# Kernel tuning notes

Measured on AMD Instinct MI355X. Metric: run time of the kernel, lower is better.

## Reference

```python
import jax, jax.numpy as jnp
import numpy as np

B, S, H = 4, 2048, 512
E, K = 8, 2
DFF = 4 * H


def setup_inputs() -> dict:
    key = jax.random.key(0)
    ks = jax.random.split(key, 6)
    x = jax.random.normal(ks[0], (B, S, H), dtype=jnp.float32)
    gate_W = jax.random.normal(ks[1], (H, E), dtype=jnp.float32) * 0.02
    gate_b = jnp.zeros((E,), dtype=jnp.float32)
    # Stacked expert params; Linear stored as [in, out] so y = x @ W + b
    W1 = jax.random.normal(ks[2], (E, H, DFF), dtype=jnp.float32) * 0.02
    b1 = jnp.zeros((E, DFF), dtype=jnp.float32)
    W2 = jax.random.normal(ks[3], (E, DFF, H), dtype=jnp.float32) * 0.02
    b2 = jnp.zeros((E, H), dtype=jnp.float32)
    return {"x": x, "gate_W": gate_W, "gate_b": gate_b,
            "W1": W1, "b1": b1, "W2": W2, "b2": b2}


def reference(x, gate_W, gate_b, W1, b1, W2, b2):
    bsz, seq, hid = x.shape
    flat = x.reshape(-1, hid)                       # [T, H]
    T = flat.shape[0]
    gate_logits = flat @ gate_W + gate_b            # [T, E]
    topk_vals, topk_idx = jax.lax.top_k(gate_logits, K)   # [T, K]
    topk_w = jax.nn.softmax(topk_vals, axis=-1)      # softmax over selected logits only

    # Scatter top-k weights into a dense per-token combine matrix [T, E];
    # zero weight where a token is not routed -> identical math to masked dispatch.
    combine = jnp.zeros((T, E), dtype=flat.dtype).at[
        jnp.arange(T)[:, None], topk_idx].add(topk_w)

    out_flat = jnp.zeros_like(flat)
    for e in range(E):  # fixed small loop over structurally distinct experts
        h = jax.nn.gelu(flat @ W1[e] + b1[e], approximate=False) @ W2[e] + b2[e]
        out_flat = out_flat + h * combine[:, e:e + 1]
    out = out_flat.reshape(bsz, seq, hid)

    probs = jax.nn.softmax(gate_logits, axis=-1).mean(axis=0)   # [E]
    l_aux = jnp.sum(probs * probs) * E
    expert_counts = jnp.zeros((E,), dtype=jnp.float32).at[
        topk_idx.reshape(-1)].add(1.0)
    return out, l_aux, expert_counts
```

## Files before the change

### kernel.cpp

```cpp
#include <hip/hip_runtime.h>
#include <math.h>

#define TOK 8192
#define HD  512
#define NE  8
#define DFF 2048

typedef __attribute__((ext_vector_type(8))) short bf16x8;
typedef __attribute__((ext_vector_type(4))) float floatx4;

__device__ inline unsigned short f2bf(float f) {
    union { float f; unsigned u; } v; v.f = f;
    unsigned r = v.u + 0x7FFFu + ((v.u >> 16) & 1u);
    return (unsigned short)(r >> 16);
}

__device__ inline float gelu_exact(float v) {
    return 0.5f * v * (1.f + erff(v * 0.70710678118654752f));
}

typedef __attribute__((address_space(1))) const unsigned int glb_u32;
typedef __attribute__((address_space(3))) unsigned int lds_u32;
__device__ __forceinline__ void gload16(const unsigned short* g, unsigned short* l) {
    __builtin_amdgcn_global_load_lds((glb_u32*)g, (lds_u32*)l, 16, 0, 0);
}

__global__ __launch_bounds__(256) void prep_kernel(
    const float* __restrict__ x, const float* __restrict__ gW, const float* __restrict__ gb,
    const float* __restrict__ W1, const float* __restrict__ W2,
    int* __restrict__ seg_count, float* __restrict__ probs_sum,
    int* __restrict__ seg_token, float* __restrict__ seg_w,
    unsigned short* __restrict__ xb,
    unsigned short* __restrict__ W1t, unsigned short* __restrict__ W2t)
{
    __shared__ __align__(16) char shraw[16896];
    int bid = blockIdx.x;
    int tid = threadIdx.x;

    if (bid >= 32) {
        int b = bid - 32;
        float (*tile)[65] = (float(*)[65])shraw;
        int z = b >> 8, rem = b & 255;
        int xq = rem & 31, yq = rem >> 5;
        const float* src; unsigned short* dst; int C, R, cb, rb;
        if (z < NE) {
            src = W1 + (size_t)z * HD * DFF; dst = W1t + (size_t)z * HD * DFF;
            R = HD; C = DFF; cb = xq; rb = yq;
        } else {
            int e = z - NE;
            src = W2 + (size_t)e * DFF * HD; dst = W2t + (size_t)e * DFF * HD;
            R = DFF; C = HD; cb = yq; rb = xq;
        }
        int c0 = cb * 64, r0 = rb * 64;
        int lc = tid & 63, lrw = tid >> 6;
        #pragma unroll
        for (int rr = lrw; rr < 64; rr += 4)
            tile[rr][lc] = src[(size_t)(r0 + rr) * C + c0 + lc];
        __syncthreads();
        #pragma unroll
        for (int cc = lrw; cc < 64; cc += 4)
            dst[(size_t)(c0 + cc) * R + r0 + lc] = f2bf(tile[lc][cc]);
        return;
    }

    float* sW    = (float*)shraw;
    float* psum  = (float*)(shraw + 16384);
    int*   lcount = (int*)(shraw + 16448);
    int*   lbase  = (int*)(shraw + 16512);

    for (int i = tid; i < HD * NE; i += 256) sW[i] = gW[i];
    if (tid < NE) { psum[tid] = 0.f; lcount[tid] = 0; }
    __syncthreads();

    int t = bid * 256 + tid;
    float logit[NE];
    #pragma unroll
    for (int e = 0; e < NE; e++) logit[e] = gb[e];

    const float4* xr4 = reinterpret_cast<const float4*>(x + (size_t)t * HD);
    ushort4* xbw = reinterpret_cast<ushort4*>(xb + (size_t)t * HD);
    for (int j4 = 0; j4 < HD / 4; j4++) {
        float4 xv = xr4[j4];
        int j = j4 * 4;
        ushort4 o; o.x = f2bf(xv.x); o.y = f2bf(xv.y); o.z = f2bf(xv.z); o.w = f2bf(xv.w);
        xbw[j4] = o;
        #pragma unroll
        for (int e = 0; e < NE; e++) {
            logit[e] += xv.x * sW[(j + 0) * NE + e] + xv.y * sW[(j + 1) * NE + e]
                      + xv.z * sW[(j + 2) * NE + e] + xv.w * sW[(j + 3) * NE + e];
        }
    }

    float mx = logit[0];
    #pragma unroll
    for (int e = 1; e < NE; e++) mx = fmaxf(mx, logit[e]);
    float pe[NE]; float s = 0.f;
    #pragma unroll
    for (int e = 0; e < NE; e++) { pe[e] = expf(logit[e] - mx); s += pe[e]; }
    float inv = 1.f / s;
    int l = tid & 63;
    #pragma unroll
    for (int e = 0; e < NE; e++) {
        float v = pe[e] * inv;
        for (int off = 32; off; off >>= 1) v += __shfl_down(v, off);
        if (l == 0) atomicAdd(&psum[e], v);
    }

    int i0 = 0; float v0 = logit[0];
    #pragma unroll
    for (int e = 1; e < NE; e++) if (logit[e] > v0) { v0 = logit[e]; i0 = e; }
    int i1 = -1; float v1 = -3.4e38f;
    #pragma unroll
    for (int e = 0; e < NE; e++) if (e != i0 && logit[e] > v1) { v1 = logit[e]; i1 = e; }
    float e1 = expf(v1 - v0);
    float w0 = 1.f / (1.f + e1);
    float w1 = e1 / (1.f + e1);

    int r0 = atomicAdd(&lcount[i0], 1);
    int r1 = atomicAdd(&lcount[i1], 1);
    __syncthreads();
    if (tid < NE) lbase[tid] = atomicAdd(&seg_count[tid], lcount[tid]);
    __syncthreads();
    int p0 = lbase[i0] + r0;
    seg_token[i0 * TOK + p0] = t; seg_w[i0 * TOK + p0] = w0;
    int p1 = lbase[i1] + r1;
    seg_token[i1 * TOK + p1] = t; seg_w[i1 * TOK + p1] = w1;

    __syncthreads();
    if (tid < NE) atomicAdd(&probs_sum[tid], psum[tid]);
}

#define TM  128
#define TN  128
#define BK  64

__global__ __launch_bounds__(256) void gemm1_kernel(
    const unsigned short* __restrict__ xb,
    const unsigned short* __restrict__ W1t,
    const float* __restrict__ bias1,
    const int* __restrict__ seg_count, const float* __restrict__ probs_sum,
    const int* __restrict__ seg_token,
    unsigned short* __restrict__ hbuf,
    float* __restrict__ out_tail)
{
    int bid = blockIdx.x;
    int tid = threadIdx.x;

    if (bid == 0) {
        if (tid < NE) out_tail[1 + tid] = (float)seg_count[tid];
        else if (tid == 64) {
            float s = 0.f;
            #pragma unroll
            for (int e2 = 0; e2 < NE; e2++) {
                float p = probs_sum[e2] * (1.f / (float)TOK);
                s += p * p;
            }
            out_tail[0] = s * (float)NE;
        }
    }

    int e  = bid & 7;
    int r2 = bid >> 3;
    int nb = r2 & 15;
    int mb = r2 >> 4;
    int cnt = seg_count[e];
    if (mb * TM >= cnt) return;
    int off_e = 0;
    #pragma unroll
    for (int ee = 0; ee < NE; ee++) if (ee < e) off_e += (seg_count[ee] + 127) & ~127;
    int hb = off_e + mb * TM;

    __shared__ __align__(16) unsigned short smem[2][2][TM * 64];
    __shared__ int tok_s[TM];
    if (tid < TM) {
        int gi = mb * TM + tid;
        tok_s[tid] = seg_token[e * TOK + ((gi < cnt) ? gi : 0)];
    }
    __syncthreads();

    int w = tid >> 6, l = tid & 63;
    int lr = l & 15, crow = (l >> 4) * 4;
    int wm = (w & 1) * 64, wn = (w >> 1) * 64;
    const unsigned short* w1e = W1t + (size_t)e * DFF * HD + (size_t)(nb * TN) * HD;

    int srow = w * 32 + (l >> 3);
    int c8   = (l & 7) ^ ((l >> 3) & 7);
    unsigned aofs[4], bofs[4];
    #pragma unroll
    for (int s = 0; s < 4; s++) {
        int r = srow + 8 * s;
        aofs[s] = (unsigned)tok_s[r] * HD + (unsigned)(c8 * 8);
        bofs[s] = (unsigned)(r * HD) + (unsigned)(c8 * 8);
    }
    int slot0 = (((l >> 4) ^ (lr & 7)) << 3);
    int slot1 = slot0 ^ 32;

    floatx4 acc[4][4];
    #pragma unroll
    for (int i = 0; i < 4; i++)
        #pragma unroll
        for (int j = 0; j < 4; j++) acc[i][j] = (floatx4){0.f, 0.f, 0.f, 0.f};

    #pragma unroll
    for (int s = 0; s < 4; s++) {
        gload16(xb  + aofs[s], &smem[0][0][(w * 32 + 8 * s) * 64]);
        gload16(w1e + bofs[s], &smem[0][1][(w * 32 + 8 * s) * 64]);
    }
    int buf = 0;
    for (int k0 = 0; k0 < HD; k0 += BK) {
        __syncthreads();
        const unsigned short* A = smem[buf][0];
        const unsigned short* B = smem[buf][1];
        bf16x8 a0[4], b0[4], a1[4], b1f[4];
        #pragma unroll
        for (int i = 0; i < 4; i++) {
            a0[i]  = *(const bf16x8*)&A[(wm + 16 * i + lr) * 64 + slot0];
            a1[i]  = *(const bf16x8*)&A[(wm + 16 * i + lr) * 64 + slot1];
            b0[i]  = *(const bf16x8*)&B[(wn + 16 * i + lr) * 64 + slot0];
            b1f[i] = *(const bf16x8*)&B[(wn + 16 * i + lr) * 64 + slot1];
        }
        int nk = k0 + BK;
        if (nk < HD) {
            int nbf = buf ^ 1;
            #pragma unroll
            for (int s = 0; s < 4; s++) {
                gload16(xb  + aofs[s] + nk, &smem[nbf][0][(w * 32 + 8 * s) * 64]);
                gload16(w1e + bofs[s] + nk, &smem[nbf][1][(w * 32 + 8 * s) * 64]);
            }
        }
        #pragma unroll
        for (int i = 0; i < 4; i++)
            #pragma unroll
            for (int j = 0; j < 4; j++)
                acc[i][j] = __builtin_amdgcn_mfma_f32_16x16x32_bf16(a0[i], b0[j], acc[i][j], 0, 0, 0);
        #pragma unroll
        for (int i = 0; i < 4; i++)
            #pragma unroll
            for (int j = 0; j < 4; j++)
                acc[i][j] = __builtin_amdgcn_mfma_f32_16x16x32_bf16(a1[i], b1f[j], acc[i][j], 0, 0, 0);
        buf ^= 1;
    }
    __syncthreads();

    unsigned short* scr = &smem[0][0][0] + w * 64 * 72;
    #pragma unroll
    for (int j = 0; j < 4; j++) {
        float b1v = bias1[e * DFF + nb * TN + wn + 16 * j + lr];
        #pragma unroll
        for (int i = 0; i < 4; i++)
            #pragma unroll
            for (int rr = 0; rr < 4; rr++)
                scr[(16 * i + crow + rr) * 72 + 16 * j + lr] = f2bf(gelu_exact(acc[i][j][rr] + b1v));
    }
    __syncthreads();
    int lh = l >> 3, ll = l & 7;
    #pragma unroll
    for (int k = 0; k < 8; k++) {
        uint4 v = *(const uint4*)&scr[(8 * k + lh) * 72 + ll * 8];
        int grow = hb + wm + 8 * k + lh;
        *(uint4*)&hbuf[(size_t)grow * DFF + nb * TN + wn + ll * 8] = v;
    }
}

__global__ __launch_bounds__(256) void gemm2_kernel(
    const unsigned short* __restrict__ hbuf,
    const unsigned short* __restrict__ W2t,
    const float* __restrict__ b2,
    const int* __restrict__ seg_count, const int* __restrict__ seg_token,
    const float* __restrict__ seg_w,
    float* __restrict__ out)
{
    int bid = blockIdx.x;
    int tid = threadIdx.x;
    int e  = bid & 7;
    int r2 = bid >> 3;
    int nb = r2 & 3;
    int mb = r2 >> 2;
    int cnt = seg_count[e];
    if (mb * TM >= cnt) return;
    int off_e = 0;
    #pragma unroll
    for (int ee = 0; ee < NE; ee++) if (ee < e) off_e += (seg_count[ee] + 127) & ~127;
    int hb = off_e + mb * TM;

    __shared__ __align__(16) unsigned short smem[2][2][TM * 64];
    __shared__ int   tok_s[TM];
    __shared__ float wgt_s[TM];
    if (tid < TM) {
        int gi = mb * TM + tid;
        tok_s[tid] = seg_token[e * TOK + ((gi < cnt) ? gi : 0)];
        wgt_s[tid] = (gi < cnt) ? seg_w[e * TOK + gi] : 0.f;
    }
    __syncthreads();

    int w = tid >> 6, l = tid & 63;
    int lr = l & 15, crow = (l >> 4) * 4;
    int wm = (w & 1) * 64, wn = (w >> 1) * 64;
    const unsigned short* w2e = W2t + (size_t)e * HD * DFF + (size_t)(nb * TN) * DFF;

    int srow = w * 32 + (l >> 3);
    int c8   = (l & 7) ^ ((l >> 3) & 7);
    unsigned aofs[4], bofs[4];
    #pragma unroll
    for (int s = 0; s < 4; s++) {
        int r = srow + 8 * s;
        aofs[s] = (unsigned)((hb + r) * DFF) + (unsigned)(c8 * 8);
        bofs[s] = (unsigned)(r * DFF) + (unsigned)(c8 * 8);
    }
    int slot0 = (((l >> 4) ^ (lr & 7)) << 3);
    int slot1 = slot0 ^ 32;

    floatx4 acc[4][4];
    #pragma unroll
    for (int i = 0; i < 4; i++)
        #pragma unroll
        for (int j = 0; j < 4; j++) acc[i][j] = (floatx4){0.f, 0.f, 0.f, 0.f};

    #pragma unroll
    for (int s = 0; s < 4; s++) {
        gload16(hbuf + aofs[s], &smem[0][0][(w * 32 + 8 * s) * 64]);
        gload16(w2e  + bofs[s], &smem[0][1][(w * 32 + 8 * s) * 64]);
    }
    int buf = 0;
    for (int k0 = 0; k0 < DFF; k0 += BK) {
        __syncthreads();
        const unsigned short* A = smem[buf][0];
        const unsigned short* B = smem[buf][1];
        bf16x8 a0[4], b0[4], a1[4], b1f[4];
        #pragma unroll
        for (int i = 0; i < 4; i++) {
            a0[i]  = *(const bf16x8*)&A[(wm + 16 * i + lr) * 64 + slot0];
            a1[i]  = *(const bf16x8*)&A[(wm + 16 * i + lr) * 64 + slot1];
            b0[i]  = *(const bf16x8*)&B[(wn + 16 * i + lr) * 64 + slot0];
            b1f[i] = *(const bf16x8*)&B[(wn + 16 * i + lr) * 64 + slot1];
        }
        int nk = k0 + BK;
        if (nk < DFF) {
            int nbf = buf ^ 1;
            #pragma unroll
            for (int s = 0; s < 4; s++) {
                gload16(hbuf + aofs[s] + nk, &smem[nbf][0][(w * 32 + 8 * s) * 64]);
                gload16(w2e  + bofs[s] + nk, &smem[nbf][1][(w * 32 + 8 * s) * 64]);
            }
        }
        #pragma unroll
        for (int i = 0; i < 4; i++)
            #pragma unroll
            for (int j = 0; j < 4; j++)
                acc[i][j] = __builtin_amdgcn_mfma_f32_16x16x32_bf16(a0[i], b0[j], acc[i][j], 0, 0, 0);
        #pragma unroll
        for (int i = 0; i < 4; i++)
            #pragma unroll
            for (int j = 0; j < 4; j++)
                acc[i][j] = __builtin_amdgcn_mfma_f32_16x16x32_bf16(a1[i], b1f[j], acc[i][j], 0, 0, 0);
        buf ^= 1;
    }

    #pragma unroll
    for (int j = 0; j < 4; j++) {
        int n = nb * TN + wn + 16 * j + lr;
        float b2v = b2[e * HD + n];
        #pragma unroll
        for (int i = 0; i < 4; i++)
            #pragma unroll
            for (int rr = 0; rr < 4; rr++) {
                int m = wm + 16 * i + crow + rr;
                atomicAdd(&out[(size_t)tok_s[m] * HD + n], (acc[i][j][rr] + b2v) * wgt_s[m]);
            }
    }
}

#define BMT 64
#define FK  64
#define XS_LD 520
#define HS_LD 72

__global__ __launch_bounds__(256, 2) void ffn_fused_fallback(
    const unsigned short* __restrict__ xb,
    const unsigned short* __restrict__ W1t, const float* __restrict__ b1,
    const unsigned short* __restrict__ W2t, const float* __restrict__ b2,
    const int* __restrict__ seg_count, const int* __restrict__ seg_token,
    const float* __restrict__ seg_w, float* __restrict__ out)
{
    int bid = blockIdx.x;
    int e = bid & 7;
    int g = bid >> 3;
    int cnt = seg_count[e];
    int n0 = g * BMT;
    if (n0 >= cnt) return;
    int rows = min(BMT, cnt - n0);

    __shared__ unsigned short xs[BMT * XS_LD];
    __shared__ unsigned short hs[BMT * HS_LD];
    __shared__ int   tok_s[BMT];
    __shared__ float wgt_s[BMT];

    int tid = threadIdx.x;
    if (tid < BMT) {
        int idx = (tid < rows) ? (n0 + tid) : n0;
        tok_s[tid] = seg_token[e * TOK + idx];
        wgt_s[tid] = (tid < rows) ? seg_w[e * TOK + idx] : 0.f;
    }
    __syncthreads();
    {
        int r = tid >> 2, q = tid & 3;
        const uint4* src = (const uint4*)(xb + (size_t)tok_s[r] * HD) + q * 16;
        uint4* dst = (uint4*)&xs[(size_t)r * XS_LD + q * 128];
        #pragma unroll
        for (int i = 0; i < 16; i++) dst[i] = src[i];
    }
    __syncthreads();

    int w = tid >> 6, l = tid & 63;
    int lr = l & 15, lk = (l >> 4) * 8, crow = (l >> 4) * 4;

    const unsigned short* w1e = W1t + (size_t)e * DFF * HD;
    const unsigned short* w2e = W2t + (size_t)e * HD * DFF;

    floatx4 acc2[4][8];
    #pragma unroll
    for (int i = 0; i < 4; i++)
        #pragma unroll
        for (int j = 0; j < 8; j++) acc2[i][j] = (floatx4){0.f, 0.f, 0.f, 0.f};

    for (int fc = 0; fc < DFF; fc += FK) {
        floatx4 acc1[4];
        #pragma unroll
        for (int t = 0; t < 4; t++) acc1[t] = (floatx4){0.f, 0.f, 0.f, 0.f};
        const unsigned short* w1c = w1e + (size_t)fc * HD;
        for (int ks = 0; ks < HD; ks += 32) {
            bf16x8 a = *(const bf16x8*)&xs[(16 * w + lr) * XS_LD + ks + lk];
            #pragma unroll
            for (int t = 0; t < 4; t++) {
                bf16x8 b = *(const bf16x8*)(w1c + (size_t)(16 * t + lr) * HD + ks + lk);
                acc1[t] = __builtin_amdgcn_mfma_f32_16x16x32_bf16(a, b, acc1[t], 0, 0, 0);
            }
        }
        __syncthreads();
        #pragma unroll
        for (int t = 0; t < 4; t++) {
            float b1v = b1[e * DFF + fc + 16 * t + lr];
            #pragma unroll
            for (int r = 0; r < 4; r++)
                hs[(16 * w + crow + r) * HS_LD + 16 * t + lr] = f2bf(gelu_exact(acc1[t][r] + b1v));
        }
        __syncthreads();
        #pragma unroll
        for (int ks = 0; ks < FK; ks += 32) {
            bf16x8 af[4];
            #pragma unroll
            for (int i = 0; i < 4; i++) af[i] = *(const bf16x8*)&hs[(16 * i + lr) * HS_LD + ks + lk];
            #pragma unroll 4
            for (int j = 0; j < 8; j++) {
                bf16x8 b = *(const bf16x8*)(w2e + (size_t)(128 * w + 16 * j + lr) * DFF + fc + ks + lk);
                #pragma unroll
                for (int i = 0; i < 4; i++)
                    acc2[i][j] = __builtin_amdgcn_mfma_f32_16x16x32_bf16(af[i], b, acc2[i][j], 0, 0, 0);
            }
        }
    }
    #pragma unroll
    for (int j = 0; j < 8; j++) {
        int n = 128 * w + 16 * j + lr;
        float b2v = b2[e * HD + n];
        #pragma unroll
        for (int i = 0; i < 4; i++)
            #pragma unroll
            for (int r = 0; r < 4; r++) {
                int m = 16 * i + crow + r;
                atomicAdd(&out[(size_t)tok_s[m] * HD + n], (acc2[i][j][r] + b2v) * wgt_s[m]);
            }
    }
}

__global__ void finalize_kernel(const int* __restrict__ seg_count,
                                const float* __restrict__ probs_sum,
                                float* __restrict__ out_tail)
{
    int tid = threadIdx.x;
    if (tid < NE) out_tail[1 + tid] = (float)seg_count[tid];
    if (tid == 0) {
        float s = 0.f;
        #pragma unroll
        for (int e = 0; e < NE; e++) {
            float p = probs_sum[e] * (1.f / (float)TOK);
            s += p * p;
        }
        out_tail[0] = s * (float)NE;
    }
}

extern "C" void kernel_launch(void* const* d_in, const int* in_sizes, int n_in,
                              void* d_out, int out_size, void* d_ws, size_t ws_size,
                              hipStream_t stream)
{
    const float* x  = (const float*)d_in[0];
    const float* gW = (const float*)d_in[1];
    const float* gb = (const float*)d_in[2];
    const float* W1 = (const float*)d_in[3];
    const float* b1 = (const float*)d_in[4];
    const float* W2 = (const float*)d_in[5];
    const float* b2 = (const float*)d_in[6];
    float* out = (float*)d_out;

    char* ws = (char*)d_ws;
    int*   seg_count = (int*)ws;
    float* probs_sum = (float*)(ws + 32);
    int*   seg_token = (int*)(ws + 262144);
    float* seg_w     = (float*)(ws + 262144 + (size_t)NE * TOK * 4);
    unsigned short* xb   = (unsigned short*)(ws + (1u  << 20));
    unsigned short* W1t  = (unsigned short*)(ws + (16u << 20));
    unsigned short* W2t  = (unsigned short*)(ws + (32u << 20));
    unsigned short* hbuf = (unsigned short*)(ws + (48u << 20));

    const size_t WS_SPLIT = (size_t)(48u << 20) + (size_t)17408 * DFF * 2;

    hipMemsetAsync(d_ws, 0, 64, stream);
    hipMemsetAsync(d_out, 0, (size_t)TOK * HD * sizeof(float), stream);

    prep_kernel<<<4128, 256, 0, stream>>>(x, gW, gb, W1, W2,
                                          seg_count, probs_sum, seg_token, seg_w,
                                          xb, W1t, W2t);

    if (ws_size >= WS_SPLIT) {
        gemm1_kernel<<<NE * (DFF / TN) * 64, 256, 0, stream>>>(
            xb, W1t, b1, seg_count, probs_sum, seg_token, hbuf,
            out + (size_t)TOK * HD);
        gemm2_kernel<<<NE * (HD / TN) * 64, 256, 0, stream>>>(
            hbuf, W2t, b2, seg_count, seg_token, seg_w, out);
    } else {
        finalize_kernel<<<1, 64, 0, stream>>>(seg_count, probs_sum, out + (size_t)TOK * HD);
        ffn_fused_fallback<<<(TOK / BMT) * NE, 256, 0, stream>>>(
            xb, W1t, b1, W2t, b2, seg_count, seg_token, seg_w, out);
    }
}
```

Measured before the change: 351.8 us.

## Use triple-buffered BK=32 pipeline with explicit vmcnt waits in expert GEMMs

Both expert GEMM kernels switch from a double-buffered BK=64 loop to a three-stage LDS ring with BK=32. Each step waits only on the older global-to-LDS loads via s_waitcnt vmcnt and a raw s_barrier, then prefetches two stages ahead. MFMA issue is raised with s_setprio. The goal is to hide global load latency and cut barrier stalls, at the cost of twice as many iterations. The XOR swizzle is dropped for a plain 32-wide row layout, which may add LDS bank conflicts.

```diff
diff --git a/kernel.cpp b/kernel.cpp
--- a/kernel.cpp
+++ b/kernel.cpp
@@ -132,7 +132,7 @@
 
 #define TM  128
 #define TN  128
-#define BK  64
+#define BK  32
 
 __global__ __launch_bounds__(256) void gemm1_kernel(
     const unsigned short* __restrict__ xb,
@@ -170,7 +170,7 @@
     for (int ee = 0; ee < NE; ee++) if (ee < e) off_e += (seg_count[ee] + 127) & ~127;
     int hb = off_e + mb * TM;
 
-    __shared__ __align__(16) unsigned short smem[2][2][TM * 64];
+    __shared__ __align__(16) unsigned short smem[3][2][TM * BK];
     __shared__ int tok_s[TM];
     if (tid < TM) {
         int gi = mb * TM + tid;
@@ -181,19 +181,16 @@
     int w = tid >> 6, l = tid & 63;
     int lr = l & 15, crow = (l >> 4) * 4;
     int wm = (w & 1) * 64, wn = (w >> 1) * 64;
+    int kq = (l >> 4) * 8;
     const unsigned short* w1e = W1t + (size_t)e * DFF * HD + (size_t)(nb * TN) * HD;
 
-    int srow = w * 32 + (l >> 3);
-    int c8   = (l & 7) ^ ((l >> 3) & 7);
-    unsigned aofs[4], bofs[4];
-    #pragma unroll
-    for (int s = 0; s < 4; s++) {
-        int r = srow + 8 * s;
-        aofs[s] = (unsigned)tok_s[r] * HD + (unsigned)(c8 * 8);
-        bofs[s] = (unsigned)(r * HD) + (unsigned)(c8 * 8);
-    }
-    int slot0 = (((l >> 4) ^ (lr & 7)) << 3);
-    int slot1 = slot0 ^ 32;
+    unsigned aofs[2], bofs[2];
+    #pragma unroll
+    for (int s = 0; s < 2; s++) {
+        int r = w * 32 + s * 16 + (l >> 2);
+        aofs[s] = (unsigned)tok_s[r] * HD + (unsigned)((l & 3) * 8);
+        bofs[s] = (unsigned)(r * HD) + (unsigned)((l & 3) * 8);
+    }
 
     floatx4 acc[4][4];
     #pragma unroll
@@ -202,43 +199,44 @@
         for (int j = 0; j < 4; j++) acc[i][j] = (floatx4){0.f, 0.f, 0.f, 0.f};
 
     #pragma unroll
-    for (int s = 0; s < 4; s++) {
-        gload16(xb  + aofs[s], &smem[0][0][(w * 32 + 8 * s) * 64]);
-        gload16(w1e + bofs[s], &smem[0][1][(w * 32 + 8 * s) * 64]);
-    }
-    int buf = 0;
-    for (int k0 = 0; k0 < HD; k0 += BK) {
-        __syncthreads();
-        const unsigned short* A = smem[buf][0];
-        const unsigned short* B = smem[buf][1];
-        bf16x8 a0[4], b0[4], a1[4], b1f[4];
-        #pragma unroll
-        for (int i = 0; i < 4; i++) {
-            a0[i]  = *(const bf16x8*)&A[(wm + 16 * i + lr) * 64 + slot0];
-            a1[i]  = *(const bf16x8*)&A[(wm + 16 * i + lr) * 64 + slot1];
-            b0[i]  = *(const bf16x8*)&B[(wn + 16 * i + lr) * 64 + slot0];
-            b1f[i] = *(const bf16x8*)&B[(wn + 16 * i + lr) * 64 + slot1];
-        }
-        int nk = k0 + BK;
-        if (nk < HD) {
-            int nbf = buf ^ 1;
-            #pragma unroll
-            for (int s = 0; s < 4; s++) {
-                gload16(xb  + aofs[s] + nk, &smem[nbf][0][(w * 32 + 8 * s) * 64]);
-                gload16(w1e + bofs[s] + nk, &smem[nbf][1][(w * 32 + 8 * s) * 64]);
-            }
-        }
+    for (int p = 0; p < 2; p++)
+        #pragma unroll
+        for (int s = 0; s < 2; s++) {
+            gload16(xb  + aofs[s] + p * BK, &smem[p][0][(w * 32 + s * 16) * BK]);
+            gload16(w1e + bofs[s] + p * BK, &smem[p][1][(w * 32 + s * 16) * BK]);
+        }
+
+    const int NIT = HD / BK;
+    int rb = 0;
+    for (int k = 0; k < NIT; ++k) {
+        if (k + 1 < NIT) asm volatile("s_waitcnt vmcnt(4)" ::: "memory");
+        else             asm volatile("s_waitcnt vmcnt(0)" ::: "memory");
+        __builtin_amdgcn_s_barrier();
+        asm volatile("" ::: "memory");
+        if (k + 2 < NIT) {
+            int ib = (rb == 0) ? 2 : rb - 1;
+            int ko = (k + 2) * BK;
+            #pragma unroll
+            for (int s = 0; s < 2; s++) {
+                gload16(xb  + aofs[s] + ko, &smem[ib][0][(w * 32 + s * 16) * BK]);
+                gload16(w1e + bofs[s] + ko, &smem[ib][1][(w * 32 + s * 16) * BK]);
+            }
+        }
+        const unsigned short* A = smem[rb][0];
+        const unsigned short* B = smem[rb][1];
+        bf16x8 a[4], b[4];
+        #pragma unroll
+        for (int i = 0; i < 4; i++) a[i] = *(const bf16x8*)&A[(wm + 16 * i + lr) * BK + kq];
+        #pragma unroll
+        for (int j = 0; j < 4; j++) b[j] = *(const bf16x8*)&B[(wn + 16 * j + lr) * BK + kq];
+        __builtin_amdgcn_s_setprio(1);
         #pragma unroll
         for (int i = 0; i < 4; i++)
             #pragma unroll
             for (int j = 0; j < 4; j++)
-                acc[i][j] = __builtin_amdgcn_mfma_f32_16x16x32_bf16(a0[i], b0[j], acc[i][j], 0, 0, 0);
-        #pragma unroll
-        for (int i = 0; i < 4; i++)
-            #pragma unroll
-            for (int j = 0; j < 4; j++)
-                acc[i][j] = __builtin_amdgcn_mfma_f32_16x16x32_bf16(a1[i], b1f[j], acc[i][j], 0, 0, 0);
-        buf ^= 1;
+                acc[i][j] = __builtin_amdgcn_mfma_f32_16x16x32_bf16(a[i], b[j], acc[i][j], 0, 0, 0);
+        __builtin_amdgcn_s_setprio(0);
+        rb = (rb == 2) ? 0 : rb + 1;
     }
     __syncthreads();
 
@@ -283,7 +281,7 @@
     for (int ee = 0; ee < NE; ee++) if (ee < e) off_e += (seg_count[ee] + 127) & ~127;
     int hb = off_e + mb * TM;
 
-    __shared__ __align__(16) unsigned short smem[2][2][TM * 64];
+    __shared__ __align__(16) unsigned short smem[3][2][TM * BK];
     __shared__ int   tok_s[TM];
     __shared__ float wgt_s[TM];
     if (tid < TM) {
@@ -296,19 +294,16 @@
     int w = tid >> 6, l = tid & 63;
     int lr = l & 15, crow = (l >> 4) * 4;
     int wm = (w & 1) * 64, wn = (w >> 1) * 64;
+    int kq = (l >> 4) * 8;
     const unsigned short* w2e = W2t + (size_t)e * HD * DFF + (size_t)(nb * TN) * DFF;
 
-    int srow = w * 32 + (l >> 3);
-    int c8   = (l & 7) ^ ((l >> 3) & 7);
-    unsigned aofs[4], bofs[4];
-    #pragma unroll
-    for (int s = 0; s < 4; s++) {
-        int r = srow + 8 * s;
-        aofs[s] = (unsigned)((hb + r) * DFF) + (unsigned)(c8 * 8);
-        bofs[s] = (unsigned)(r * DFF) + (unsigned)(c8 * 8);
-    }
-    int slot0 = (((l >> 4) ^ (lr & 7)) << 3);
-    int slot1 = slot0 ^ 32;
+    unsigned aofs[2], bofs[2];
+    #pragma unroll
+    for (int s = 0; s < 2; s++) {
+        int r = w * 32 + s * 16 + (l >> 2);
+        aofs[s] = (unsigned)((hb + r) * DFF) + (unsigned)((l & 3) * 8);
+        bofs[s] = (unsigned)(r * DFF) + (unsigned)((l & 3) * 8);
+    }
 
     floatx4 acc[4][4];
     #pragma unroll
@@ -317,43 +312,44 @@
         for (int j = 0; j < 4; j++) acc[i][j] = (floatx4){0.f, 0.f, 0.f, 0.f};
 
     #pragma unroll
-    for (int s = 0; s < 4; s++) {
-        gload16(hbuf + aofs[s], &smem[0][0][(w * 32 + 8 * s) * 64]);
-        gload16(w2e  + bofs[s], &smem[0][1][(w * 32 + 8 * s) * 64]);
-    }
-    int buf = 0;
-    for (int k0 = 0; k0 < DFF; k0 += BK) {
-        __syncthreads();
-        const unsigned short* A = smem[buf][0];
-        const unsigned short* B = smem[buf][1];
-        bf16x8 a0[4], b0[4], a1[4], b1f[4];
-        #pragma unroll
-        for (int i = 0; i < 4; i++) {
-            a0[i]  = *(const bf16x8*)&A[(wm + 16 * i + lr) * 64 + slot0];
-            a1[i]  = *(const bf16x8*)&A[(wm + 16 * i + lr) * 64 + slot1];
-            b0[i]  = *(const bf16x8*)&B[(wn + 16 * i + lr) * 64 + slot0];
-            b1f[i] = *(const bf16x8*)&B[(wn + 16 * i + lr) * 64 + slot1];
-        }
-        int nk = k0 + BK;
-        if (nk < DFF) {
-            int nbf = buf ^ 1;
-            #pragma unroll
-            for (int s = 0; s < 4; s++) {
-                gload16(hbuf + aofs[s] + nk, &smem[nbf][0][(w * 32 + 8 * s) * 64]);
-                gload16(w2e  + bofs[s] + nk, &smem[nbf][1][(w * 32 + 8 * s) * 64]);
-            }
-        }
+    for (int p = 0; p < 2; p++)
+        #pragma unroll
+        for (int s = 0; s < 2; s++) {
+            gload16(hbuf + aofs[s] + p * BK, &smem[p][0][(w * 32 + s * 16) * BK]);
+            gload16(w2e  + bofs[s] + p * BK, &smem[p][1][(w * 32 + s * 16) * BK]);
+        }
+
+    const int NIT = DFF / BK;
+    int rb = 0;
+    for (int k = 0; k < NIT; ++k) {
+        if (k + 1 < NIT) asm volatile("s_waitcnt vmcnt(4)" ::: "memory");
+        else             asm volatile("s_waitcnt vmcnt(0)" ::: "memory");
+        __builtin_amdgcn_s_barrier();
+        asm volatile("" ::: "memory");
+        if (k + 2 < NIT) {
+            int ib = (rb == 0) ? 2 : rb - 1;
+            int ko = (k + 2) * BK;
+            #pragma unroll
+            for (int s = 0; s < 2; s++) {
+                gload16(hbuf + aofs[s] + ko, &smem[ib][0][(w * 32 + s * 16) * BK]);
+                gload16(w2e  + bofs[s] + ko, &smem[ib][1][(w * 32 + s * 16) * BK]);
+            }
+        }
+        const unsigned short* A = smem[rb][0];
+        const unsigned short* B = smem[rb][1];
+        bf16x8 a[4], b[4];
+        #pragma unroll
+        for (int i = 0; i < 4; i++) a[i] = *(const bf16x8*)&A[(wm + 16 * i + lr) * BK + kq];
+        #pragma unroll
+        for (int j = 0; j < 4; j++) b[j] = *(const bf16x8*)&B[(wn + 16 * j + lr) * BK + kq];
+        __builtin_amdgcn_s_setprio(1);
         #pragma unroll
         for (int i = 0; i < 4; i++)
             #pragma unroll
             for (int j = 0; j < 4; j++)
-                acc[i][j] = __builtin_amdgcn_mfma_f32_16x16x32_bf16(a0[i], b0[j], acc[i][j], 0, 0, 0);
-        #pragma unroll
-        for (int i = 0; i < 4; i++)
-            #pragma unroll
-            for (int j = 0; j < 4; j++)
-                acc[i][j] = __builtin_amdgcn_mfma_f32_16x16x32_bf16(a1[i], b1f[j], acc[i][j], 0, 0, 0);
-        buf ^= 1;
+                acc[i][j] = __builtin_amdgcn_mfma_f32_16x16x32_bf16(a[i], b[j], acc[i][j], 0, 0, 0);
+        __builtin_amdgcn_s_setprio(0);
+        rb = (rb == 2) ? 0 : rb + 1;
     }
 
     #pragma unroll
```

After: 349.6 us. Within noise of the previous version (-0.6%).
